# Optimization experiments

Hardware: AMD Instinct MI355X
Metric: run time of the kernel (lower is better)

The kernel has to match this reference:

```python
import jax, jax.numpy as jnp
import numpy as np

INTERVAL = 4
UPSCALE = 4
K = 3              # sample_size
SAMPLERS = 3
Q = 2 ** INTERVAL                 # 16
L = 2 ** (8 - INTERVAL) + 1       # 17
PAD = K - 1
B, H, W = 4, 512, 512

_STRIDES = np.array([L ** 3, L ** 2, L, 1], dtype=np.int32)


def ste_round(x):
    # straight-through round (round_func in the torch code)
    return x + jax.lax.stop_gradient(jnp.round(x) - x)


def fix_weight(w):
    return jnp.clip(ste_round(w * 127.0), -127.0, 127.0)


def sample(img, sw, sb):
    # unfold(K, K-1) + conv-per-patch + fold is exactly a VALID conv.
    # img: (B,1,h+PAD,w+PAD); sw: (4,1,K,K) -> a,b,c,d each (B,1,h,w)
    out = jax.lax.conv_general_dilated(img, sw, (1, 1), 'VALID',
        dimension_numbers=('NCHW', 'OIHW', 'NCHW')) + sb[None, :, None, None]
    return out[:, 0:1], out[:, 1:2], out[:, 2:3], out[:, 3:4]


def interp(lut, res_w, sw, sb, scale, img_in, prev_img):
    # InterpTorchBatch: 4D simplex interpolation into the quantized LUT.
    # Sorted-simplex form is equivalent to the 24-case masked torch code
    # (ties yield zero-weight terms, so tie ordering is irrelevant).
    w = fix_weight(lut)                                       # (L^4, scale*scale)
    a, b, c, d = sample(img_in, sw, sb)
    if prev_img is not None:
        rw = jnp.clip(res_w, 0.0, 1.0)
        pa, pb, pc, pd = sample(prev_img, sw, sb)
        a = rw[0, 0] * pa + (1.0 - rw[0, 0]) * a
        b = rw[0, 1] * pb + (1.0 - rw[0, 1]) * b
        c = rw[1, 0] * pc + (1.0 - rw[1, 0]) * c
        d = rw[1, 1] * pd + (1.0 - rw[1, 1]) * d
    vals = jnp.concatenate([a, b, c, d], axis=1).transpose(0, 2, 3, 1)   # (B,h,w,4)
    lo = jnp.floor_divide(vals, float(Q)).astype(jnp.int32)
    f = jnp.mod(vals, float(Q))
    order = jnp.argsort(-f, axis=-1)                          # fractional parts, descending
    fs = jnp.take_along_axis(f, order, axis=-1)
    strides = jnp.asarray(_STRIDES)
    base = jnp.sum(lo * strides, axis=-1)                     # flat index of p0000
    inc = jnp.cumsum(strides[order], axis=-1)
    verts = jnp.concatenate([base[..., None], base[..., None] + inc], axis=-1)  # (B,h,w,5)
    ws = jnp.concatenate([float(Q) - fs[..., :1], fs[..., :-1] - fs[..., 1:], fs[..., -1:]], axis=-1)
    p = w[verts]                                              # gather: (B,h,w,5,scale*scale)
    out = jnp.einsum('bhwv,bhwvk->bhwk', ws, p) / float(Q)
    bb, hh, ww, _ = out.shape
    out = out.reshape(bb, hh, ww, scale, scale).transpose(0, 1, 3, 2, 4)
    return out.reshape(bb, 1, hh * scale, ww * scale)


def _pad_rot(x, r):
    return jnp.pad(jnp.rot90(x, r, axes=(2, 3)),
                   ((0, 0), (0, 0), (0, PAD), (0, PAD)), mode='edge')


def rotate_input(lut, scale, sw, sb, x, res_w, prev_x):
    pred = jnp.zeros((), jnp.float32)
    for r in range(4):
        pr = None if prev_x is None else _pad_rot(prev_x, r)
        pred = pred + jnp.rot90(
            interp(lut, res_w, sw, sb, scale, _pad_rot(x, r), pr),
            (4 - r) % 4, axes=(2, 3))
        pred = ste_round(pred)
    return pred


def autolut_forward(x, lut0, lut1, samp0, samp1, sbias0, sbias1, resw1):
    x = x * 255.0
    # stage 0: scale 1, no residual, bias 127
    pred = 0.0
    for s in range(SAMPLERS):
        pred = pred + rotate_input(lut0[s], 1, samp0[s], sbias0[s], x, None, None)
    prev_x = x
    x = ste_round(jnp.clip(pred / (SAMPLERS * 4.0) + 127.0, 0.0, 255.0))
    # stage 1 (last): upscale, residual blend with previous stage input
    pred = 0.0
    for s in range(SAMPLERS):
        pred = pred + rotate_input(lut1[s], UPSCALE, samp1[s], sbias1[s], x, resw1[s], prev_x)
    x = ste_round(jnp.clip(pred / float(SAMPLERS), 0.0, 255.0))
    return x / 255.0   # phase == 'train'


def setup_inputs() -> dict:
    key = jax.random.key(0)
    ks = jax.random.split(key, 6)
    x = jax.random.uniform(ks[0], (B, 1, H, W), dtype=jnp.float32)
    lut0 = jax.random.uniform(ks[1], (SAMPLERS, L ** 4, 1), jnp.float32, -1.0, 1.0)
    lut1 = jax.random.uniform(ks[2], (SAMPLERS, L ** 4, UPSCALE * UPSCALE), jnp.float32, -1.0, 1.0)

    def mk_sampler(k):
        w = jax.random.normal(k, (SAMPLERS, 4, 1, K, K), dtype=jnp.float32)
        # convex combination of patch pixels -> sampled values stay in [0,255]
        return jax.nn.softmax(w.reshape(SAMPLERS, 4, -1), axis=-1).reshape(SAMPLERS, 4, 1, K, K)

    samp0 = mk_sampler(ks[3])
    samp1 = mk_sampler(ks[4])
    sbias0 = jnp.zeros((SAMPLERS, 4), jnp.float32)
    sbias1 = jnp.zeros((SAMPLERS, 4), jnp.float32)
    resw1 = jax.random.uniform(ks[5], (SAMPLERS, 2, 2), dtype=jnp.float32)
    return {"x": x, "lut0": lut0, "lut1": lut1, "samp0": samp0, "samp1": samp1,
            "sbias0": sbias0, "sbias1": sbias1, "resw1": resw1}


def reference(x, lut0, lut1, samp0, samp1, sbias0, sbias1, resw1):
    return autolut_forward(x, lut0, lut1, samp0, samp1, sbias0, sbias1, resw1)
```

## Files before the change

### kernel.cpp

```cpp
#include <hip/hip_runtime.h>
#include <math.h>

static constexpr int B_ = 4;
static constexpr int N_ = 512;
static constexpr int N4_ = 2048;
static constexpr int NPIX = B_ * N_ * N_;
static constexpr int LUT_ROWS = 83521;
static constexpr int SPAD = 83584;
static constexpr int ST0 = 4913, ST1 = 289, ST2 = 17, ST3 = 1;

__device__ __forceinline__ float fixw(float v) {
    v = rintf(v * 127.0f);
    return fminf(fmaxf(v, -127.0f), 127.0f);
}

__global__ void fix_lut0_kernel(const float* __restrict__ in, char* __restrict__ out) {
    int t = blockIdx.x * blockDim.x + threadIdx.x;
    int s = blockIdx.y;
    if (t < LUT_ROWS) out[(size_t)s * SPAD + t] = (char)(int)fixw(in[(size_t)s * LUT_ROWS + t]);
}

__global__ void fix_lut1_kernel(const float4* __restrict__ in, uchar4* __restrict__ out, int n4) {
    int t = blockIdx.x * blockDim.x + threadIdx.x;
    if (t < n4) {
        float4 v = in[t];
        uchar4 o;
        o.x = (unsigned char)((int)fixw(v.x) + 127);
        o.y = (unsigned char)((int)fixw(v.y) + 127);
        o.z = (unsigned char)((int)fixw(v.z) + 127);
        o.w = (unsigned char)((int)fixw(v.w) + 127);
        out[t] = o;
    }
}

struct Simplex {
    int v[5];
    float w[5];
};

__device__ __forceinline__ double pack_key(float f, unsigned stride) {
    unsigned long long u = ((unsigned long long)__float_as_uint(f) << 32) | stride;
    return __longlong_as_double((long long)u);
}
__device__ __forceinline__ float key_f(double k) {
    return __uint_as_float((unsigned)((unsigned long long)__double_as_longlong(k) >> 32));
}
__device__ __forceinline__ int key_s(double k) {
    return (int)(unsigned)__double_as_longlong(k);
}

__device__ __forceinline__ Simplex simplex4(float a, float b, float c, float d) {
    float fl0 = floorf(a * 0.0625f), fl1 = floorf(b * 0.0625f),
          fl2 = floorf(c * 0.0625f), fl3 = floorf(d * 0.0625f);
    float f0 = a - 16.0f * fl0, f1 = b - 16.0f * fl1,
          f2 = c - 16.0f * fl2, f3 = d - 16.0f * fl3;
    int l0 = min(max((int)fl0, 0), 15);
    int l1 = min(max((int)fl1, 0), 15);
    int l2 = min(max((int)fl2, 0), 15);
    int l3 = min(max((int)fl3, 0), 15);
    double k0 = pack_key(f0, (unsigned)ST0);
    double k1 = pack_key(f1, (unsigned)ST1);
    double k2 = pack_key(f2, (unsigned)ST2);
    double k3 = pack_key(f3, (unsigned)ST3);
#define CSWD(X, Y) { double mx_ = fmax(X, Y); Y = fmin(X, Y); X = mx_; }
    CSWD(k0, k1) CSWD(k2, k3) CSWD(k0, k2) CSWD(k1, k3) CSWD(k1, k2)
#undef CSWD
    Simplex s;
    s.v[0] = l0 * ST0 + l1 * ST1 + l2 * ST2 + l3;
    s.v[1] = s.v[0] + key_s(k0);
    s.v[2] = s.v[1] + key_s(k1);
    s.v[3] = s.v[2] + key_s(k2);
    s.v[4] = s.v[3] + key_s(k3);
    float g0 = key_f(k0), g1 = key_f(k1), g2 = key_f(k2), g3 = key_f(k3);
    s.w[0] = (16.0f - g0) * 0.0625f;
    s.w[1] = (g0 - g1) * 0.0625f;
    s.w[2] = (g1 - g2) * 0.0625f;
    s.w[3] = (g2 - g3) * 0.0625f;
    s.w[4] = g3 * 0.0625f;
    return s;
}

__device__ __forceinline__ bool tap_for_r(int r, int a, int c, int& di, int& dj) {
    if (r == 0) { di = a - 2; dj = c - 2; return (a >= 2) && (c >= 2); }
    if (r == 1) { di = 2 - c; dj = a - 2; return (a >= 2) && (c <= 2); }
    if (r == 2) { di = 2 - a; dj = 2 - c; return (a <= 2) && (c <= 2); }
    di = c - 2; dj = 2 - a; return (a <= 2) && (c >= 2);
}

__device__ __forceinline__ void acc4u(unsigned int q, float wv, float* oc) {
    oc[0] = fmaf(wv, (float)(q & 0xffu), oc[0]);
    oc[1] = fmaf(wv, (float)((q >> 8) & 0xffu), oc[1]);
    oc[2] = fmaf(wv, (float)((q >> 16) & 0xffu), oc[2]);
    oc[3] = fmaf(wv, (float)(q >> 24), oc[3]);
}

__global__ __launch_bounds__(1024, 4) void stage0_kernel(
    const float* __restrict__ x,
    const char* __restrict__ lut0q,
    const float* __restrict__ samp0,
    const float* __restrict__ sbias0,
    float* __restrict__ x1)
{
    __shared__ char luts[SPAD];

    int b    = blockIdx.x >> 8;
    int tile = blockIdx.x & 255;
    int i = ((tile >> 4) << 5) + (threadIdx.x >> 5);
    int j = ((tile & 15) << 5) + (threadIdx.x & 31);
    const float* xb = x + (size_t)b * N_ * N_;

    float vals[3][4][4];
    #pragma unroll
    for (int s = 0; s < 3; ++s)
        #pragma unroll
        for (int r = 0; r < 4; ++r)
            #pragma unroll
            for (int ch = 0; ch < 4; ++ch) vals[s][r][ch] = 0.0f;
    #pragma unroll
    for (int a = 0; a < 5; ++a) {
        int ri = min(max(i - 2 + a, 0), N_ - 1);
        const float* row = xb + ri * N_;
        #pragma unroll
        for (int c = 0; c < 5; ++c) {
            int ci = min(max(j - 2 + c, 0), N_ - 1);
            float px = row[ci] * 255.0f;
            #pragma unroll
            for (int r = 0; r < 4; ++r) {
                int di, dj;
                if (tap_for_r(r, a, c, di, dj)) {
                    #pragma unroll
                    for (int s = 0; s < 3; ++s)
                        #pragma unroll
                        for (int ch = 0; ch < 4; ++ch)
                            vals[s][r][ch] += samp0[s * 36 + ch * 9 + di * 3 + dj] * px;
                }
            }
        }
    }

    float pred = 0.0f;
    #pragma unroll
    for (int s = 0; s < 3; ++s) {
        __syncthreads();
        {
            const int4* src = (const int4*)(lut0q + (size_t)s * SPAD);
            int4* dst = (int4*)luts;
            for (int u = threadIdx.x; u < SPAD / 16; u += 1024) dst[u] = src[u];
        }
        __syncthreads();

        const float* sb = sbias0 + s * 4;
        float acc = 0.0f;
        #pragma unroll
        for (int r = 0; r < 4; ++r) {
            Simplex sx = simplex4(vals[s][r][0] + sb[0], vals[s][r][1] + sb[1],
                                  vals[s][r][2] + sb[2], vals[s][r][3] + sb[3]);
            float p0 = (float)luts[sx.v[0]];
            float p1 = (float)luts[sx.v[1]];
            float p2 = (float)luts[sx.v[2]];
            float p3 = (float)luts[sx.v[3]];
            float p4 = (float)luts[sx.v[4]];
            float o = sx.w[0] * p0 + sx.w[1] * p1 + sx.w[2] * p2
                    + sx.w[3] * p3 + sx.w[4] * p4;
            acc = rintf(acc + o);
        }
        pred += acc;
    }
    x1[(size_t)b * N_ * N_ + i * N_ + j] =
        rintf(fminf(fmaxf(pred / 12.0f + 127.0f, 0.0f), 255.0f));
}

__global__ __launch_bounds__(256, 1) void stage1_kernel(
    const float* __restrict__ x,
    const float* __restrict__ x1,
    const unsigned char* __restrict__ lut1q,
    const float* __restrict__ samp1,
    const float* __restrict__ sbias1,
    const float* __restrict__ resw1,
    float* __restrict__ out)
{
    int b    = blockIdx.x >> 10;
    int tile = blockIdx.x & 1023;
    int i = ((tile >> 5) << 4) + (threadIdx.x >> 4);
    int j = ((tile & 31) << 4) + (threadIdx.x & 15);
    const float* xb  = x  + (size_t)b * N_ * N_;
    const float* x1b = x1 + (size_t)b * N_ * N_;

    float tot[16];
    #pragma unroll
    for (int k = 0; k < 16; ++k) tot[k] = 0.0f;

    for (int s = 0; s < 3; ++s) {
        const float* w  = samp1 + s * 36;
        const unsigned char* lut = lut1q + (size_t)s * LUT_ROWS * 16;
        float rws[4];
        #pragma unroll
        for (int ch = 0; ch < 4; ++ch)
            rws[ch] = fminf(fmaxf(resw1[s * 4 + ch], 0.0f), 1.0f);

        float vals[4][4];
        #pragma unroll
        for (int r = 0; r < 4; ++r)
            #pragma unroll
            for (int ch = 0; ch < 4; ++ch) vals[r][ch] = sbias1[s * 4 + ch];

        #pragma unroll
        for (int a = 0; a < 5; ++a) {
            int ri = min(max(i - 2 + a, 0), N_ - 1);
            const float* r1 = x1b + ri * N_;
            const float* r0 = xb + ri * N_;
            #pragma unroll
            for (int c = 0; c < 5; ++c) {
                int ci = min(max(j - 2 + c, 0), N_ - 1);
                float pc = r1[ci];
                float dq = r0[ci] * 255.0f - pc;
                float q[4];
                #pragma unroll
                for (int ch = 0; ch < 4; ++ch)
                    q[ch] = fmaf(rws[ch], dq, pc);
                #pragma unroll
                for (int r = 0; r < 4; ++r) {
                    int di, dj;
                    if (tap_for_r(r, a, c, di, dj)) {
                        #pragma unroll
                        for (int ch = 0; ch < 4; ++ch)
                            vals[r][ch] += w[ch * 9 + di * 3 + dj] * q[ch];
                    }
                }
            }
        }

        Simplex sx[4];
        #pragma unroll
        for (int r = 0; r < 4; ++r)
            sx[r] = simplex4(vals[r][0], vals[r][1], vals[r][2], vals[r][3]);

        uint4 g[4][5];
        #pragma unroll
        for (int r = 0; r < 4; ++r)
            #pragma unroll
            for (int v = 0; v < 5; ++v)
                g[r][v] = *(const uint4*)(lut + (size_t)sx[r].v[v] * 16);

        float acc[16];
        #pragma unroll
        for (int k = 0; k < 16; ++k) acc[k] = 0.0f;

        #pragma unroll
        for (int r = 0; r < 4; ++r) {
            #pragma unroll
            for (int v = 0; v < 5; ++v)
                asm volatile("" : "+v"(g[r][v].x), "+v"(g[r][v].y),
                                  "+v"(g[r][v].z), "+v"(g[r][v].w));
            float oc[16];
            #pragma unroll
            for (int k = 0; k < 16; ++k) oc[k] = 0.0f;
            #pragma unroll
            for (int v = 0; v < 5; ++v) {
                float wv = sx[r].w[v];
                acc4u(g[r][v].x, wv, oc);
                acc4u(g[r][v].y, wv, oc + 4);
                acc4u(g[r][v].z, wv, oc + 8);
                acc4u(g[r][v].w, wv, oc + 12);
            }
            float S = sx[r].w[0] + sx[r].w[1] + sx[r].w[2] + sx[r].w[3] + sx[r].w[4];
            float bias = 127.0f * S;
            #pragma unroll
            for (int k = 0; k < 16; ++k) oc[k] -= bias;
            #pragma unroll
            for (int u = 0; u < 4; ++u)
                #pragma unroll
                for (int v2 = 0; v2 < 4; ++v2) {
                    int k = 4 * u + v2;
                    int c = (r == 0) ? (4 * u + v2)
                          : (r == 1) ? (4 * (3 - v2) + u)
                          : (r == 2) ? (4 * (3 - u) + (3 - v2))
                                     : (4 * v2 + (3 - u));
                    acc[k] = rintf(acc[k] + oc[c]);
                }
        }
        #pragma unroll
        for (int k = 0; k < 16; ++k) tot[k] += acc[k];
    }

    float* ob = out + (size_t)b * N4_ * N4_ + (size_t)(i * 4) * N4_ + (j * 4);
    #pragma unroll
    for (int u = 0; u < 4; ++u) {
        float4 val;
        val.x = rintf(fminf(fmaxf(tot[4 * u + 0] / 3.0f, 0.0f), 255.0f)) * (1.0f / 255.0f);
        val.y = rintf(fminf(fmaxf(tot[4 * u + 1] / 3.0f, 0.0f), 255.0f)) * (1.0f / 255.0f);
        val.z = rintf(fminf(fmaxf(tot[4 * u + 2] / 3.0f, 0.0f), 255.0f)) * (1.0f / 255.0f);
        val.w = rintf(fminf(fmaxf(tot[4 * u + 3] / 3.0f, 0.0f), 255.0f)) * (1.0f / 255.0f);
        *(float4*)(ob + (size_t)u * N4_) = val;
    }
}

extern "C" void kernel_launch(void* const* d_in, const int* in_sizes, int n_in,
                              void* d_out, int out_size, void* d_ws, size_t ws_size,
                              hipStream_t stream) {
    const float* x      = (const float*)d_in[0];
    const float* lut0   = (const float*)d_in[1];
    const float* lut1   = (const float*)d_in[2];
    const float* samp0  = (const float*)d_in[3];
    const float* samp1  = (const float*)d_in[4];
    const float* sbias0 = (const float*)d_in[5];
    const float* sbias1 = (const float*)d_in[6];
    const float* resw1  = (const float*)d_in[7];
    float* out = (float*)d_out;
    char* ws   = (char*)d_ws;

    const int N_L1 = 3 * LUT_ROWS * 16;
    size_t off_x1 = 0;
    size_t off_l0 = (size_t)NPIX * sizeof(float);
    size_t off_l1 = (off_l0 + (size_t)3 * SPAD + 15) & ~(size_t)15;

    float* x1 = (float*)(ws + off_x1);
    char* l0q = ws + off_l0;
    unsigned char* l1q = (unsigned char*)(ws + off_l1);

    const int threads = 256;

    dim3 g0((LUT_ROWS + threads - 1) / threads, 3);
    fix_lut0_kernel<<<g0, threads, 0, stream>>>(lut0, l0q);
    fix_lut1_kernel<<<(N_L1 / 4 + threads - 1) / threads, threads, 0, stream>>>(
        (const float4*)lut1, (uchar4*)l1q, N_L1 / 4);
    stage0_kernel<<<NPIX / 1024, 1024, 0, stream>>>(x, l0q, samp0, sbias0, x1);
    stage1_kernel<<<NPIX / threads, threads, 0, stream>>>(x, x1, l1q, samp1, sbias1, resw1, out);
}
```

Before: 281.1 us.

## Prefetch next sampler LUT into registers and batch LDS gathers in stage0

Stage0 now loads each sampler's quantized LUT slice from global memory into per-thread int4 staging registers one step ahead. The next slice's global loads are issued while the current slice's lookups run, so the copy into shared memory only stores from registers. The simplex lookups are also grouped in pairs, with the LDS gathers for two positions issued together and asm barriers keeping them ahead of the arithmetic. The cost is about 24 extra VGPRs per thread at 1024 threads per block, which may cause register pressure or spills under the existing launch bounds.

```diff
diff --git a/kernel.cpp b/kernel.cpp
--- a/kernel.cpp
+++ b/kernel.cpp
@@ -8,6 +8,7 @@
 static constexpr int LUT_ROWS = 83521;
 static constexpr int SPAD = 83584;
 static constexpr int ST0 = 4913, ST1 = 289, ST2 = 17, ST3 = 1;
+static constexpr int SCHUNK = SPAD / 16;
 
 __device__ __forceinline__ float fixw(float v) {
     v = rintf(v * 127.0f);
@@ -107,7 +108,16 @@
     int tile = blockIdx.x & 255;
     int i = ((tile >> 4) << 5) + (threadIdx.x >> 5);
     int j = ((tile & 15) << 5) + (threadIdx.x & 31);
+    const int tid = threadIdx.x;
     const float* xb = x + (size_t)b * N_ * N_;
+
+    int4 stg[6];
+    {
+        const int4* src = (const int4*)lut0q;
+        #pragma unroll
+        for (int k = 0; k < 5; ++k) stg[k] = src[tid + k * 1024];
+        if (tid < SCHUNK - 5120) stg[5] = src[tid + 5120];
+    }
 
     float vals[3][4][4];
     #pragma unroll
@@ -143,26 +153,49 @@
     for (int s = 0; s < 3; ++s) {
         __syncthreads();
         {
-            const int4* src = (const int4*)(lut0q + (size_t)s * SPAD);
             int4* dst = (int4*)luts;
-            for (int u = threadIdx.x; u < SPAD / 16; u += 1024) dst[u] = src[u];
+            #pragma unroll
+            for (int k = 0; k < 5; ++k) dst[tid + k * 1024] = stg[k];
+            if (tid < SCHUNK - 5120) dst[tid + 5120] = stg[5];
         }
         __syncthreads();
+
+        if (s < 2) {
+            const int4* src = (const int4*)(lut0q + (size_t)(s + 1) * SPAD);
+            #pragma unroll
+            for (int k = 0; k < 5; ++k) stg[k] = src[tid + k * 1024];
+            if (tid < SCHUNK - 5120) stg[5] = src[tid + 5120];
+        }
 
         const float* sb = sbias0 + s * 4;
         float acc = 0.0f;
         #pragma unroll
-        for (int r = 0; r < 4; ++r) {
-            Simplex sx = simplex4(vals[s][r][0] + sb[0], vals[s][r][1] + sb[1],
-                                  vals[s][r][2] + sb[2], vals[s][r][3] + sb[3]);
-            float p0 = (float)luts[sx.v[0]];
-            float p1 = (float)luts[sx.v[1]];
-            float p2 = (float)luts[sx.v[2]];
-            float p3 = (float)luts[sx.v[3]];
-            float p4 = (float)luts[sx.v[4]];
-            float o = sx.w[0] * p0 + sx.w[1] * p1 + sx.w[2] * p2
-                    + sx.w[3] * p3 + sx.w[4] * p4;
-            acc = rintf(acc + o);
+        for (int rp = 0; rp < 2; ++rp) {
+            Simplex sx0 = simplex4(vals[s][2 * rp + 0][0] + sb[0],
+                                   vals[s][2 * rp + 0][1] + sb[1],
+                                   vals[s][2 * rp + 0][2] + sb[2],
+                                   vals[s][2 * rp + 0][3] + sb[3]);
+            Simplex sx1 = simplex4(vals[s][2 * rp + 1][0] + sb[0],
+                                   vals[s][2 * rp + 1][1] + sb[1],
+                                   vals[s][2 * rp + 1][2] + sb[2],
+                                   vals[s][2 * rp + 1][3] + sb[3]);
+            float p0[5], p1[5];
+            #pragma unroll
+            for (int v = 0; v < 5; ++v) p0[v] = (float)luts[sx0.v[v]];
+            #pragma unroll
+            for (int v = 0; v < 5; ++v) p1[v] = (float)luts[sx1.v[v]];
+
+            asm volatile("" : "+v"(p0[0]), "+v"(p0[1]), "+v"(p0[2]),
+                              "+v"(p0[3]), "+v"(p0[4]));
+            float o0 = sx0.w[0] * p0[0] + sx0.w[1] * p0[1] + sx0.w[2] * p0[2]
+                     + sx0.w[3] * p0[3] + sx0.w[4] * p0[4];
+            acc = rintf(acc + o0);
+
+            asm volatile("" : "+v"(p1[0]), "+v"(p1[1]), "+v"(p1[2]),
+                              "+v"(p1[3]), "+v"(p1[4]));
+            float o1 = sx1.w[0] * p1[0] + sx1.w[1] * p1[1] + sx1.w[2] * p1[2]
+                     + sx1.w[3] * p1[3] + sx1.w[4] * p1[4];
+            acc = rintf(acc + o1);
         }
         pred += acc;
     }
```

Result: slower. 334.5 us (+19.0%).
